# Optimization experiments

Measured on AMD Instinct MI355X. Metric: run time of the kernel, lower is better.

The kernel has to match this reference:

```python
import jax, jax.numpy as jnp
import numpy as np

R_MAX = 32
S_MAX = 2
N_RES_BINS = 2 * R_MAX + 2      # 66 (shared by residue and token one-hots)
N_CHAIN_BINS = 2 * S_MAX + 2    # 6
NO_BINS = N_RES_BINS + N_RES_BINS + 1 + N_CHAIN_BINS  # 139
C_Z = 128


def setup_inputs() -> dict:
    key = jax.random.key(0)
    ks = jax.random.split(key, 6)
    B, N = 1, 1024
    asym_id = jax.random.randint(ks[0], (B, N), 0, 8, dtype=jnp.int32)
    residue_index = jnp.sort(jax.random.randint(ks[1], (B, N), 0, 1024, dtype=jnp.int32), axis=-1)
    entity_id = jax.random.randint(ks[2], (B, N), 0, 4, dtype=jnp.int32)
    token_index = jnp.sort(jax.random.randint(ks[3], (B, N), 0, 2048, dtype=jnp.int32), axis=-1)
    sym_id = jax.random.randint(ks[4], (B, N), 0, 4, dtype=jnp.int32)
    # Linear(no_bins, c_z, bias=False): weight shape [c_z, no_bins]
    W = jax.random.normal(ks[5], (C_Z, NO_BINS), dtype=jnp.float32) * (NO_BINS ** -0.5)
    return {
        "asym_id": asym_id,
        "residue_index": residue_index,
        "entity_id": entity_id,
        "token_index": token_index,
        "sym_id": sym_id,
        "W": W,
    }


def _rel_feat(asym_id, residue_index, entity_id, token_index, sym_id, dtype=jnp.float32):
    # pairwise [B, N, N] comparisons
    b_same_chain = asym_id[..., :, None] == asym_id[..., None, :]
    b_same_residue = residue_index[..., :, None] == residue_index[..., None, :]
    b_same_entity = entity_id[..., :, None] == entity_id[..., None, :]

    # residue-level relative position, clamped; off-chain -> sentinel bin 2*r_max+1
    d_residue = residue_index[..., :, None] - residue_index[..., None, :]
    d_residue = jnp.clip(d_residue + R_MAX, 0, 2 * R_MAX)
    d_residue = jnp.where(b_same_chain, d_residue, 2 * R_MAX + 1)
    a_rel_pos = jax.nn.one_hot(d_residue, N_RES_BINS, dtype=dtype)

    # token-level relative position within same chain & residue
    d_token = token_index[..., :, None] - token_index[..., None, :]
    d_token = jnp.clip(d_token + R_MAX, 0, 2 * R_MAX)
    d_token = jnp.where(b_same_chain & b_same_residue, d_token, 2 * R_MAX + 1)
    a_rel_token = jax.nn.one_hot(d_token, N_RES_BINS, dtype=dtype)

    # chain-level relative position within same entity
    d_chain = sym_id[..., :, None] - sym_id[..., None, :]
    d_chain = jnp.clip(d_chain + S_MAX, 0, 2 * S_MAX)
    d_chain = jnp.where(b_same_entity, d_chain, 2 * S_MAX + 1)
    a_rel_chain = jax.nn.one_hot(d_chain, N_CHAIN_BINS, dtype=dtype)

    # [B, N, N, no_bins]
    return jnp.concatenate(
        [a_rel_pos, a_rel_token, b_same_entity[..., None].astype(dtype), a_rel_chain],
        axis=-1,
    )


def reference(asym_id, residue_index, entity_id, token_index, sym_id, W):
    rel_feat = _rel_feat(asym_id, residue_index, entity_id, token_index, sym_id, W.dtype)
    # bias-free Linear: rel_feat @ W^T -> [B, N, N, c_z]
    return jnp.einsum('...b,cb->...c', rel_feat, W)
```

## Files before the change

### kernel.cpp

```cpp
#include <hip/hip_runtime.h>


#define R_MAX 32
#define NO_BINS 139
#define C_Z 128
#define C_HALF 64
#define N_MAX 1024
#define WSTRIDE 68

typedef float v4f __attribute__((ext_vector_type(4)));

__global__ __launch_bounds__(256) void relpos_kernel(
    const int* __restrict__ asym, const int* __restrict__ res,
    const int* __restrict__ ent,  const int* __restrict__ tok,
    const int* __restrict__ sym,  const float* __restrict__ W,
    float* __restrict__ out, int N)
{
    __shared__ float wt[NO_BINS * WSTRIDE];
    __shared__ int   jb_pack[N_MAX];

    const int tid   = threadIdx.x;
    const int c_off = blockIdx.x * C_HALF;
    const int i     = blockIdx.y;

    const float* __restrict__ Wr = W + (size_t)c_off * NO_BINS;
    for (int q = tid; q < (C_HALF * NO_BINS) / 4; q += 256) {
        const v4f v = *(const v4f*)(Wr + 4 * q);
        const int e = 4 * q;
#pragma unroll
        for (int k = 0; k < 4; ++k) {
            const int ee = e + k;
            const int c  = ee / NO_BINS;
            const int b  = ee - c * NO_BINS;
            wt[b * WSTRIDE + c] = v[k];
        }
    }

    const int ai = asym[i], ri = res[i], ei = ent[i], ti = tok[i], si = sym[i];

    for (int j = tid; j < N; j += 256) {
        const int rj = res[j], tj = tok[j], aj = asym[j], ej = ent[j], sj = sym[j];
        const bool sc  = (ai == aj);
        const bool sr  = (ri == rj);
        const bool seB = (ei == ej);

        int dr = min(max(ri - rj + R_MAX, 0), 2 * R_MAX);
        if (!sc) dr = 2 * R_MAX + 1;
        int dt = min(max(ti - tj + R_MAX, 0), 2 * R_MAX);
        if (!(sc && sr)) dt = 2 * R_MAX + 1;
        int dc = min(max(si - sj + 2, 0), 4);
        if (!seB) dc = 5;

        jb_pack[j] = dr | ((66 + dt) << 7) | ((133 + dc) << 15) | ((seB ? 1 : 0) << 23);
    }
    __syncthreads();

    const int c4 = (tid & 15) * 4;
    const int jl = tid >> 4;

    const v4f entv = *(const v4f*)&wt[132 * WSTRIDE + c4];

    float* po = out + ((size_t)i * N + jl) * C_Z + c_off + c4;

    for (int jb = 0; jb < N; jb += 16) {
        const int pk   = jb_pack[jb + jl];
        const int rowR = pk & 127;
        const int rowT = (pk >> 7) & 255;
        const int rowC = (pk >> 15) & 255;
        const float se = (pk >> 23) ? 1.0f : 0.0f;

        const v4f r0 = *(const v4f*)&wt[rowR * WSTRIDE + c4];
        const v4f t0 = *(const v4f*)&wt[rowT * WSTRIDE + c4];
        const v4f k0 = *(const v4f*)&wt[rowC * WSTRIDE + c4];

        v4f o;
        o.x = fmaf(se, entv.x, r0.x + t0.x + k0.x);
        o.y = fmaf(se, entv.y, r0.y + t0.y + k0.y);
        o.z = fmaf(se, entv.z, r0.z + t0.z + k0.z);
        o.w = fmaf(se, entv.w, r0.w + t0.w + k0.w);

        __builtin_nontemporal_store(o, (v4f*)po);
        po += 16 * C_Z;
    }
}

extern "C" void kernel_launch(void* const* d_in, const int* in_sizes, int n_in,
                              void* d_out, int out_size, void* d_ws, size_t ws_size,
                              hipStream_t stream) {
    const int*   asym = (const int*)d_in[0];
    const int*   res  = (const int*)d_in[1];
    const int*   ent  = (const int*)d_in[2];
    const int*   tok  = (const int*)d_in[3];
    const int*   sym  = (const int*)d_in[4];
    const float* W    = (const float*)d_in[5];
    float* out = (float*)d_out;

    const int N = in_sizes[0];
    dim3 grid(C_Z / C_HALF, N);
    relpos_kernel<<<grid, 256, 0, stream>>>(asym, res, ent, tok, sym, W, out, N);
}
```

Measured before the change: 533.8 us.

## Process four rows per block with double-buffered pair-code computation

Each block now handles four consecutive i rows instead of one. The transposed W tile is loaded into shared memory once per four rows, which cuts that load overhead. The packed bin codes for the next row are computed into a second shared buffer while the current row's outputs are written. This adds a barrier per row and reduces the grid size four-fold, which lowers parallelism across the device.

```diff
diff --git a/kernel.cpp b/kernel.cpp
--- a/kernel.cpp
+++ b/kernel.cpp
@@ -7,6 +7,7 @@
 #define C_HALF 64
 #define N_MAX 1024
 #define WSTRIDE 68
+#define IPB 4
 
 typedef float v4f __attribute__((ext_vector_type(4)));
 
@@ -17,11 +18,11 @@
     float* __restrict__ out, int N)
 {
     __shared__ float wt[NO_BINS * WSTRIDE];
-    __shared__ int   jb_pack[N_MAX];
+    __shared__ int   jb_pack[2][N_MAX];
 
     const int tid   = threadIdx.x;
     const int c_off = blockIdx.x * C_HALF;
-    const int i     = blockIdx.y;
+    const int i0    = blockIdx.y * IPB;
 
     const float* __restrict__ Wr = W + (size_t)c_off * NO_BINS;
     for (int q = tid; q < (C_HALF * NO_BINS) / 4; q += 256) {
@@ -36,51 +37,78 @@
         }
     }
 
-    const int ai = asym[i], ri = res[i], ei = ent[i], ti = tok[i], si = sym[i];
-
-    for (int j = tid; j < N; j += 256) {
-        const int rj = res[j], tj = tok[j], aj = asym[j], ej = ent[j], sj = sym[j];
-        const bool sc  = (ai == aj);
-        const bool sr  = (ri == rj);
-        const bool seB = (ei == ej);
-
-        int dr = min(max(ri - rj + R_MAX, 0), 2 * R_MAX);
-        if (!sc) dr = 2 * R_MAX + 1;
-        int dt = min(max(ti - tj + R_MAX, 0), 2 * R_MAX);
-        if (!(sc && sr)) dt = 2 * R_MAX + 1;
-        int dc = min(max(si - sj + 2, 0), 4);
-        if (!seB) dc = 5;
-
-        jb_pack[j] = dr | ((66 + dt) << 7) | ((133 + dc) << 15) | ((seB ? 1 : 0) << 23);
+    {
+        const int i = i0;
+        const int ai = asym[i], ri = res[i], ei = ent[i], ti = tok[i], si = sym[i];
+        for (int j = tid; j < N; j += 256) {
+            const int rj = res[j], tj = tok[j], aj = asym[j], ej = ent[j], sj = sym[j];
+            const bool sc  = (ai == aj);
+            const bool sr  = (ri == rj);
+            const bool seB = (ei == ej);
+            int dr = min(max(ri - rj + R_MAX, 0), 2 * R_MAX);
+            if (!sc) dr = 2 * R_MAX + 1;
+            int dt = min(max(ti - tj + R_MAX, 0), 2 * R_MAX);
+            if (!(sc && sr)) dt = 2 * R_MAX + 1;
+            int dc = min(max(si - sj + 2, 0), 4);
+            if (!seB) dc = 5;
+            jb_pack[0][j] = dr | ((66 + dt) << 7) | ((133 + dc) << 15)
+                               | ((seB ? 1 : 0) << 23);
+        }
     }
     __syncthreads();
 
     const int c4 = (tid & 15) * 4;
     const int jl = tid >> 4;
-
     const v4f entv = *(const v4f*)&wt[132 * WSTRIDE + c4];
 
-    float* po = out + ((size_t)i * N + jl) * C_Z + c_off + c4;
+    for (int k = 0; k < IPB; ++k) {
+        const int i = i0 + k;
 
-    for (int jb = 0; jb < N; jb += 16) {
-        const int pk   = jb_pack[jb + jl];
-        const int rowR = pk & 127;
-        const int rowT = (pk >> 7) & 255;
-        const int rowC = (pk >> 15) & 255;
-        const float se = (pk >> 23) ? 1.0f : 0.0f;
+        if (k + 1 < IPB) {
+            const int ii = i + 1;
+            const int ai = asym[ii], ri = res[ii], ei = ent[ii],
+                      ti = tok[ii], si = sym[ii];
+            for (int j = tid; j < N; j += 256) {
+                const int rj = res[j], tj = tok[j], aj = asym[j],
+                          ej = ent[j], sj = sym[j];
+                const bool sc  = (ai == aj);
+                const bool sr  = (ri == rj);
+                const bool seB = (ei == ej);
+                int dr = min(max(ri - rj + R_MAX, 0), 2 * R_MAX);
+                if (!sc) dr = 2 * R_MAX + 1;
+                int dt = min(max(ti - tj + R_MAX, 0), 2 * R_MAX);
+                if (!(sc && sr)) dt = 2 * R_MAX + 1;
+                int dc = min(max(si - sj + 2, 0), 4);
+                if (!seB) dc = 5;
+                jb_pack[(k + 1) & 1][j] = dr | ((66 + dt) << 7) | ((133 + dc) << 15)
+                                             | ((seB ? 1 : 0) << 23);
+            }
+        }
 
-        const v4f r0 = *(const v4f*)&wt[rowR * WSTRIDE + c4];
-        const v4f t0 = *(const v4f*)&wt[rowT * WSTRIDE + c4];
-        const v4f k0 = *(const v4f*)&wt[rowC * WSTRIDE + c4];
+        const int* __restrict__ bp = jb_pack[k & 1];
+        float* po = out + ((size_t)i * N + jl) * C_Z + c_off + c4;
 
-        v4f o;
-        o.x = fmaf(se, entv.x, r0.x + t0.x + k0.x);
-        o.y = fmaf(se, entv.y, r0.y + t0.y + k0.y);
-        o.z = fmaf(se, entv.z, r0.z + t0.z + k0.z);
-        o.w = fmaf(se, entv.w, r0.w + t0.w + k0.w);
+        for (int jb = 0; jb < N; jb += 16) {
+            const int pk   = bp[jb + jl];
+            const int rowR = pk & 127;
+            const int rowT = (pk >> 7) & 255;
+            const int rowC = (pk >> 15) & 255;
+            const float se = (pk >> 23) ? 1.0f : 0.0f;
 
-        __builtin_nontemporal_store(o, (v4f*)po);
-        po += 16 * C_Z;
+            const v4f r0 = *(const v4f*)&wt[rowR * WSTRIDE + c4];
+            const v4f t0 = *(const v4f*)&wt[rowT * WSTRIDE + c4];
+            const v4f k0 = *(const v4f*)&wt[rowC * WSTRIDE + c4];
+
+            v4f o;
+            o.x = fmaf(se, entv.x, r0.x + t0.x + k0.x);
+            o.y = fmaf(se, entv.y, r0.y + t0.y + k0.y);
+            o.z = fmaf(se, entv.z, r0.z + t0.z + k0.z);
+            o.w = fmaf(se, entv.w, r0.w + t0.w + k0.w);
+
+            __builtin_nontemporal_store(o, (v4f*)po);
+            po += 16 * C_Z;
+        }
+        __syncthreads();
     }
 }
 
@@ -96,6 +124,6 @@
     float* out = (float*)d_out;
 
     const int N = in_sizes[0];
-    dim3 grid(C_Z / C_HALF, N);
+    dim3 grid(C_Z / C_HALF, N / IPB);
     relpos_kernel<<<grid, 256, 0, stream>>>(asym, res, ent, tok, sym, W, out, N);
 }
```

New measurement: 536.0 us. About the same (+0.4%).
